# Optimization experiments

Hardware: AMD Instinct MI355X
Metric: run time of the kernel (lower is better)

Reference implementation:

```python
import math
import jax, jax.numpy as jnp
import numpy as np

EMBED_DIM = 512
NUM_HEADS = 8
HEAD_DIM = EMBED_DIM // NUM_HEADS
NUM_EDGE_TYPES = 10
N = 2048  # nodes
B = 1


def setup_inputs() -> dict:
    key = jax.random.key(0)
    ks = jax.random.split(key, 8)
    s = 1.0 / math.sqrt(EMBED_DIM)
    return {
        "query": jax.random.normal(ks[0], (N, B, EMBED_DIM), jnp.float32),
        "key": jax.random.normal(ks[1], (N, B, EMBED_DIM), jnp.float32),
        "value": jax.random.normal(ks[2], (N, B, EMBED_DIM), jnp.float32),
        "edge_id_mat": jax.random.randint(ks[3], (N, N), 0, NUM_EDGE_TYPES, jnp.int32),
        "in_proj_weight": jax.random.normal(ks[4], (3 * EMBED_DIM, EMBED_DIM), jnp.float32) * s,
        "in_proj_bias": jnp.zeros((3 * EMBED_DIM,), jnp.float32),
        "out_proj_weight": jax.random.normal(ks[5], (EMBED_DIM, EMBED_DIM), jnp.float32) * s,
        "out_proj_bias": jnp.zeros((EMBED_DIM,), jnp.float32),
        "edge_embs_K": jax.random.normal(ks[6], (NUM_EDGE_TYPES, HEAD_DIM), jnp.float32),
    }


def reference(query, key, value, edge_id_mat, in_proj_weight, in_proj_bias,
              out_proj_weight, out_proj_bias, edge_embs_K):
    L, Bsz, E = query.shape
    H, hd = NUM_HEADS, HEAD_DIM
    w_q, w_k, w_v = jnp.split(in_proj_weight, 3, axis=0)
    b_q, b_k, b_v = jnp.split(in_proj_bias, 3)
    q = query @ w_q.T + b_q   # (L, B, E)
    k = key @ w_k.T + b_k
    v = value @ w_v.T + b_v

    def split_heads(x):
        # (L, B, E) -> (B*H, L, hd)  (matches torch view(L, B*H, hd).transpose(0,1))
        return x.reshape(L, Bsz * H, hd).transpose(1, 0, 2)

    q = split_heads(q) / math.sqrt(hd)  # torch scales by sqrt(E=head_dim)
    k = split_heads(k)
    v = split_heads(v)

    attn = jnp.einsum('bnd,bmd->bnm', q, k)  # (B*H, L, L)

    # edge-type score bias: edge_attn[b,i,j] = q[b,i,:] . edge_embs_K[edge_id_mat[i,j], :]
    # computed efficiently as per-type scores then a gather (avoids (L,L,hd) tensor)
    type_scores = jnp.einsum('bnd,td->bnt', q, edge_embs_K)  # (B*H, L, T)
    idx = jnp.broadcast_to(edge_id_mat[None, :, :], attn.shape)
    edge_attn = jnp.take_along_axis(type_scores, idx, axis=2)  # (B*H, L, L)
    attn = jax.nn.softmax(attn + edge_attn, axis=-1)

    out = jnp.einsum('bnm,bmd->bnd', attn, v)           # (B*H, L, hd)
    out = out.transpose(1, 0, 2).reshape(L, Bsz, E)      # (L, B, E)
    out = out @ out_proj_weight.T + out_proj_bias
    return out
```

## Files before the change

kernel.cpp:

```cpp
#include <hip/hip_runtime.h>
#include <hip/hip_bf16.h>

#define NHEAD 8
#define SEQ   2048
#define HD    64
#define EMB   512
#define NTYPE 10
#define JSPLIT 2

#define QKV_NT (3 * EMB / 64)
#define QKV_MT (SEQ / 64)
#define QKV_BLOCKS (QKV_NT * QKV_MT)
#define PACK_BLOCKS (SEQ * SEQ / 4 / 256)

typedef unsigned short u16;
typedef __attribute__((ext_vector_type(8))) short short8;
typedef __attribute__((ext_vector_type(4))) float float4v;

union F8 { short8 v; uint4 u4; u16 us[8]; };

__device__ __forceinline__ float bf2f(u16 u){
  union { unsigned u; float f; } w; w.u = ((unsigned)u) << 16; return w.f;
}
__device__ __forceinline__ u16 f2bf(float f){
  union { float f; unsigned u; } w; w.f = f;
  unsigned u = w.u;
  u += 0x7fffu + ((u >> 16) & 1u);
  return (u16)(u >> 16);
}
__device__ __forceinline__ unsigned pk2(float a, float b){
  return (unsigned)f2bf(a) | ((unsigned)f2bf(b) << 16);
}
__device__ __forceinline__ uint4 pk8(float4 a, float4 b){
  uint4 p; p.x = pk2(a.x, a.y); p.y = pk2(a.z, a.w);
           p.z = pk2(b.x, b.y); p.w = pk2(b.z, b.w);
  return p;
}

__global__ __launch_bounds__(256) void fused_prep_gemm(
    const float* __restrict__ q, const float* __restrict__ k, const float* __restrict__ v,
    const float* __restrict__ ipw, const float* __restrict__ ipb, const int* __restrict__ eid,
    u16* __restrict__ Qs, u16* __restrict__ Kb, u16* __restrict__ Vb,
    unsigned* __restrict__ eidp)
{
  const int b = blockIdx.x;
  const int t = threadIdx.x;

  if (b >= QKV_BLOCKS) {
    const int i = (b - QKV_BLOCKS) * 256 + t;
    int4 vv = ((const int4*)eid)[i];
    eidp[i] = (unsigned)(vv.x & 0xff) | ((unsigned)(vv.y & 0xff) << 8) |
              ((unsigned)(vv.z & 0xff) << 16) | ((unsigned)(vv.w & 0xff) << 24);
    return;
  }

  __shared__ u16 As[64][40];
  __shared__ u16 Bs[64][40];

  const int nt = b % QKV_NT, mt = b / QKV_NT;
  const int n0 = nt * 64, m0 = mt * 64;
  const int z = n0 >> 9;
  const float* A = (z == 0) ? q : (z == 1) ? k : v;
  const float scale = (z == 0) ? 0.125f : 1.0f;

  const int w = t >> 6, lane = t & 63, lr = lane & 15, lg = lane >> 4;
  const int wm = w >> 1, wn = w & 1;
  const int srow = t >> 2, kb = (t & 3) * 8;

  float4v acc[2][2];
#pragma unroll
  for (int mi = 0; mi < 2; mi++)
#pragma unroll
    for (int ni = 0; ni < 2; ni++) acc[mi][ni] = (float4v){0.f, 0.f, 0.f, 0.f};

  const float* pa = A   + (size_t)(m0 + srow) * EMB + kb;
  const float* pw = ipw + (size_t)(n0 + srow) * EMB + kb;

  float4 a0 = *(const float4*)pa, a1 = *(const float4*)(pa + 4);
  float4 b0 = *(const float4*)pw, b1 = *(const float4*)(pw + 4);

  for (int k0 = 0; k0 < EMB; k0 += 32) {
    *(uint4*)&As[srow][kb] = pk8(a0, a1);
    *(uint4*)&Bs[srow][kb] = pk8(b0, b1);
    __syncthreads();
    if (k0 + 32 < EMB) {
      a0 = *(const float4*)(pa + k0 + 32); a1 = *(const float4*)(pa + k0 + 36);
      b0 = *(const float4*)(pw + k0 + 32); b1 = *(const float4*)(pw + k0 + 36);
    }
    F8 af[2], bf_[2];
#pragma unroll
    for (int mi = 0; mi < 2; mi++)
      af[mi].u4 = *(const uint4*)&As[wm * 32 + mi * 16 + lr][lg * 8];
#pragma unroll
    for (int ni = 0; ni < 2; ni++)
      bf_[ni].u4 = *(const uint4*)&Bs[wn * 32 + ni * 16 + lr][lg * 8];
#pragma unroll
    for (int mi = 0; mi < 2; mi++)
#pragma unroll
      for (int ni = 0; ni < 2; ni++)
        acc[mi][ni] = __builtin_amdgcn_mfma_f32_16x16x32_bf16(af[mi].v, bf_[ni].v, acc[mi][ni], 0, 0, 0);
    __syncthreads();
  }

  u16* O = (z == 0) ? Qs : ((z == 1) ? Kb : Vb);
#pragma unroll
  for (int mi = 0; mi < 2; mi++) {
#pragma unroll
    for (int ni = 0; ni < 2; ni++) {
      const int n = n0 + wn * 32 + ni * 16 + lr;
      const int e = n & 511, h = e >> 6, d = e & 63;
      const float bb = ipb[n];
      const int mb = m0 + wm * 32 + mi * 16 + lg * 4;
      if (z < 2) {
#pragma unroll
        for (int r = 0; r < 4; r++)
          O[((size_t)h * SEQ + mb + r) * HD + d] = f2bf((acc[mi][ni][r] + bb) * scale);
      } else {
        ushort4 pk;
        pk.x = f2bf(acc[mi][ni][0] + bb); pk.y = f2bf(acc[mi][ni][1] + bb);
        pk.z = f2bf(acc[mi][ni][2] + bb); pk.w = f2bf(acc[mi][ni][3] + bb);
        *(ushort4*)(O + ((size_t)(h * HD + d)) * SEQ + mb) = pk;
      }
    }
  }
}

__global__ __launch_bounds__(256) void attn_kernel(
    const u16* __restrict__ Qs, const u16* __restrict__ Kb, const u16* __restrict__ Vb,
    const unsigned char* __restrict__ eidp, const float* __restrict__ EK,
    float* __restrict__ Upart, float* __restrict__ mpart, float* __restrict__ lpart)
{
  __shared__ u16 Kt[64][72];
  __shared__ u16 Vt[64][72];
  __shared__ u16 Pl[4][16][72];
  __shared__ unsigned char eidt[64][64];
  __shared__ float tsl[64][13];
  __shared__ float ekl[NTYPE][64];
  __shared__ float mrow[64], lrow[64], frow[64];

  const int t = threadIdx.x;
  const int wave = t >> 6, lane = t & 63, lr = lane & 15, lg = lane >> 4;
  const int i0 = blockIdx.x * 64;
  const int h  = blockIdx.y;
  const int z  = blockIdx.z;

  for (int i = t; i < NTYPE * 64; i += 256) ekl[i >> 6][i & 63] = EK[i];
  if (t < 64) { mrow[t] = -1e30f; lrow[t] = 0.f; }
  __syncthreads();

  {
    const int row = t >> 2, tt = t & 3;
    const u16* qr = Qs + ((size_t)h * SEQ + i0 + row) * HD;
    float a0 = 0.f, a1 = 0.f, a2 = 0.f;
    for (int d0 = 0; d0 < HD; d0 += 8) {
      uint4 qq = *(const uint4*)(qr + d0);
      const u16* qu = (const u16*)&qq;
#pragma unroll
      for (int e = 0; e < 8; e++) {
        float qf = bf2f(qu[e]);
        a0 += qf * ekl[tt][d0 + e];
        a1 += qf * ekl[tt + 4][d0 + e];
        a2 += qf * ekl[(tt < 2) ? (tt + 8) : 8][d0 + e];
      }
    }
    tsl[row][tt] = a0; tsl[row][tt + 4] = a1;
    if (tt < 2) tsl[row][tt + 8] = a2;
  }

  F8 qf[2];
#pragma unroll
  for (int kc = 0; kc < 2; kc++)
    qf[kc].u4 = *(const uint4*)(Qs + ((size_t)h * SEQ + i0 + wave * 16 + lr) * HD + kc * 32 + lg * 8);

  float4v ao[4];
#pragma unroll
  for (int d = 0; d < 4; d++) ao[d] = (float4v){0.f, 0.f, 0.f, 0.f};

  const int srow = t >> 2, sdc = (t & 3) * 16;
  const int sec = sdc ^ (((t >> 4) & 3) << 4);
  const int jbase = z * (SEQ / JSPLIT);
  const int NT = (SEQ / JSPLIT) / 64;

  uint4 kp0, kp1, vp0, vp1, ep0;
  {
    const u16* kp = Kb + ((size_t)h * SEQ + jbase + srow) * HD + sdc;
    kp0 = *(const uint4*)kp; kp1 = *(const uint4*)(kp + 8);
    const u16* vp = Vb + ((size_t)(h * HD + srow)) * SEQ + jbase + sdc;
    vp0 = *(const uint4*)vp; vp1 = *(const uint4*)(vp + 8);
    ep0 = *(const uint4*)(eidp + (size_t)(i0 + srow) * SEQ + jbase + sdc);
    *(uint4*)&Kt[srow][sdc] = kp0; *(uint4*)&Kt[srow][sdc + 8] = kp1;
    *(uint4*)&Vt[srow][sdc] = vp0; *(uint4*)&Vt[srow][sdc + 8] = vp1;
    *(uint4*)&eidt[srow][sec] = ep0;
  }

  for (int jt = 0; jt < NT; jt++) {
    __syncthreads();

    if (jt + 1 < NT) {
      const int jn = jbase + (jt + 1) * 64;
      const u16* kp = Kb + ((size_t)h * SEQ + jn + srow) * HD + sdc;
      kp0 = *(const uint4*)kp; kp1 = *(const uint4*)(kp + 8);
      const u16* vp = Vb + ((size_t)(h * HD + srow)) * SEQ + jn + sdc;
      vp0 = *(const uint4*)vp; vp1 = *(const uint4*)(vp + 8);
      ep0 = *(const uint4*)(eidp + (size_t)(i0 + srow) * SEQ + jn + sdc);
    }

    float4v sacc[4];
#pragma unroll
    for (int c = 0; c < 4; c++) sacc[c] = (float4v){0.f, 0.f, 0.f, 0.f};
    __builtin_amdgcn_s_setprio(1);
#pragma unroll
    for (int kc = 0; kc < 2; kc++) {
#pragma unroll
      for (int c = 0; c < 4; c++) {
        F8 kf; kf.u4 = *(const uint4*)&Kt[c * 16 + lr][kc * 32 + lg * 8];
        sacc[c] = __builtin_amdgcn_mfma_f32_16x16x32_bf16(qf[kc].v, kf.v, sacc[c], 0, 0, 0);
      }
    }
    __builtin_amdgcn_s_setprio(0);

    float pv_[4][4];
    float rmax[4] = {-1e30f, -1e30f, -1e30f, -1e30f};
#pragma unroll
    for (int c = 0; c < 4; c++) {
      const int ec = ((c ^ lg) << 4) + lr;
#pragma unroll
      for (int r = 0; r < 4; r++) {
        const int row = wave * 16 + lg * 4 + r;
        float s = sacc[c][r] + tsl[row][eidt[row][ec]];
        pv_[c][r] = s;
        rmax[r] = fmaxf(rmax[r], s);
      }
    }
#pragma unroll
    for (int mm = 1; mm < 16; mm <<= 1) {
#pragma unroll
      for (int r = 0; r < 4; r++) rmax[r] = fmaxf(rmax[r], __shfl_xor(rmax[r], mm));
    }
    float mnew[4], fct[4], rsum[4] = {0.f, 0.f, 0.f, 0.f};
#pragma unroll
    for (int r = 0; r < 4; r++) {
      const int row = wave * 16 + lg * 4 + r;
      const float mo = mrow[row];
      mnew[r] = fmaxf(mo, rmax[r]);
      fct[r] = __expf(mo - mnew[r]);
    }
#pragma unroll
    for (int c = 0; c < 4; c++) {
#pragma unroll
      for (int r = 0; r < 4; r++) {
        float p = __expf(pv_[c][r] - mnew[r]);
        pv_[c][r] = p;
        rsum[r] += p;
      }
    }
#pragma unroll
    for (int mm = 1; mm < 16; mm <<= 1) {
#pragma unroll
      for (int r = 0; r < 4; r++) rsum[r] += __shfl_xor(rsum[r], mm);
    }
    if (lr == 0) {
#pragma unroll
      for (int r = 0; r < 4; r++) {
        const int row = wave * 16 + lg * 4 + r;
        mrow[row] = mnew[r];
        lrow[row] = lrow[row] * fct[r] + rsum[r];
        frow[row] = fct[r];
      }
    }
#pragma unroll
    for (int c = 0; c < 4; c++) {
#pragma unroll
      for (int r = 0; r < 4; r++)
        Pl[wave][lg * 4 + r][c * 16 + lr] = f2bf(pv_[c][r]);
    }
    const float fo = frow[wave * 16 + lr];
#pragma unroll
    for (int d = 0; d < 4; d++) {
#pragma unroll
      for (int r = 0; r < 4; r++) ao[d][r] *= fo;
    }
    __builtin_amdgcn_s_setprio(1);
#pragma unroll
    for (int kc = 0; kc < 2; kc++) {
      F8 pf; pf.u4 = *(const uint4*)&Pl[wave][lr][kc * 32 + lg * 8];
#pragma unroll
      for (int db = 0; db < 4; db++) {
        F8 vf; vf.u4 = *(const uint4*)&Vt[db * 16 + lr][kc * 32 + lg * 8];
        ao[db] = __builtin_amdgcn_mfma_f32_16x16x32_bf16(vf.v, pf.v, ao[db], 0, 0, 0);
      }
    }
    __builtin_amdgcn_s_setprio(0);

    __syncthreads();
    if (jt + 1 < NT) {
      *(uint4*)&Kt[srow][sdc] = kp0; *(uint4*)&Kt[srow][sdc + 8] = kp1;
      *(uint4*)&Vt[srow][sdc] = vp0; *(uint4*)&Vt[srow][sdc + 8] = vp1;
      *(uint4*)&eidt[srow][sec] = ep0;
    }
  }

  {
    const size_t base = (((size_t)z * NHEAD + h) * SEQ + i0) * HD;
#pragma unroll
    for (int db = 0; db < 4; db++) {
#pragma unroll
      for (int r = 0; r < 4; r++) {
        const int d = db * 16 + lg * 4 + r;
        const int n = wave * 16 + lr;
        Upart[base + (size_t)n * HD + d] = ao[db][r];
      }
    }
    __syncthreads();
    if (t < 64) {
      mpart[((size_t)z * NHEAD + h) * SEQ + i0 + t] = mrow[t];
      lpart[((size_t)z * NHEAD + h) * SEQ + i0 + t] = lrow[t];
    }
  }
}

__global__ __launch_bounds__(256) void combine_outproj(
    const float* __restrict__ Upart, const float* __restrict__ mpart,
    const float* __restrict__ lpart, const float* __restrict__ opw,
    const float* __restrict__ opb, float* __restrict__ out)
{
  __shared__ u16 As[64][40];
  __shared__ u16 Bs[64][40];
  __shared__ float cw0[NHEAD][64], cw1[NHEAD][64], cwi[NHEAD][64];

  const int t = threadIdx.x;
  const int n0 = blockIdx.x * 64;
  const int m0 = blockIdx.y * 64;

  for (int idx = t; idx < NHEAD * 64; idx += 256) {
    const int hh = idx >> 6, nl = idx & 63;
    const int gn = m0 + nl;
    const float mA = mpart[((size_t)0 * NHEAD + hh) * SEQ + gn];
    const float mB = mpart[((size_t)1 * NHEAD + hh) * SEQ + gn];
    const float M = fmaxf(mA, mB);
    const float w0 = __expf(mA - M), w1 = __expf(mB - M);
    const float Ls = w0 * lpart[((size_t)0 * NHEAD + hh) * SEQ + gn] +
                     w1 * lpart[((size_t)1 * NHEAD + hh) * SEQ + gn];
    cw0[hh][nl] = w0; cw1[hh][nl] = w1; cwi[hh][nl] = 1.0f / Ls;
  }
  __syncthreads();

  const int w = t >> 6, lane = t & 63, lr = lane & 15, lg = lane >> 4;
  const int wm = w >> 1, wn = w & 1;
  const int srow = t >> 2, kb = (t & 3) * 8;

  float4v acc[2][2];
#pragma unroll
  for (int mi = 0; mi < 2; mi++)
#pragma unroll
    for (int ni = 0; ni < 2; ni++) acc[mi][ni] = (float4v){0.f, 0.f, 0.f, 0.f};

  const float* pw = opw + (size_t)(n0 + srow) * EMB + kb;

  int hcur = kb >> 6, dcur = kb & 63;
  const float* pu0 = Upart + (((size_t)0 * NHEAD + hcur) * SEQ + m0 + srow) * HD + dcur;
  const float* pu1 = Upart + (((size_t)1 * NHEAD + hcur) * SEQ + m0 + srow) * HD + dcur;
  float4 u00 = *(const float4*)pu0, u01 = *(const float4*)(pu0 + 4);
  float4 u10 = *(const float4*)pu1, u11 = *(const float4*)(pu1 + 4);
  float4 b0 = *(const float4*)pw, b1 = *(const float4*)(pw + 4);

  for (int k0 = 0; k0 < EMB; k0 += 32) {
    {
      const float w0 = cw0[hcur][srow], w1 = cw1[hcur][srow], wi = cwi[hcur][srow];
      float4 c0, c1;
      c0.x = (u00.x * w0 + u10.x * w1) * wi; c0.y = (u00.y * w0 + u10.y * w1) * wi;
      c0.z = (u00.z * w0 + u10.z * w1) * wi; c0.w = (u00.w * w0 + u10.w * w1) * wi;
      c1.x = (u01.x * w0 + u11.x * w1) * wi; c1.y = (u01.y * w0 + u11.y * w1) * wi;
      c1.z = (u01.z * w0 + u11.z * w1) * wi; c1.w = (u01.w * w0 + u11.w * w1) * wi;
      *(uint4*)&As[srow][kb] = pk8(c0, c1);
      *(uint4*)&Bs[srow][kb] = pk8(b0, b1);
    }
    __syncthreads();
    if (k0 + 32 < EMB) {
      const int e = k0 + 32 + kb;
      hcur = e >> 6; dcur = e & 63;
      const float* q0 = Upart + (((size_t)0 * NHEAD + hcur) * SEQ + m0 + srow) * HD + dcur;
      const float* q1 = Upart + (((size_t)1 * NHEAD + hcur) * SEQ + m0 + srow) * HD + dcur;
      u00 = *(const float4*)q0; u01 = *(const float4*)(q0 + 4);
      u10 = *(const float4*)q1; u11 = *(const float4*)(q1 + 4);
      b0 = *(const float4*)(pw + k0 + 32); b1 = *(const float4*)(pw + k0 + 36);
    }
    F8 af[2], bf_[2];
#pragma unroll
    for (int mi = 0; mi < 2; mi++)
      af[mi].u4 = *(const uint4*)&As[wm * 32 + mi * 16 + lr][lg * 8];
#pragma unroll
    for (int ni = 0; ni < 2; ni++)
      bf_[ni].u4 = *(const uint4*)&Bs[wn * 32 + ni * 16 + lr][lg * 8];
#pragma unroll
    for (int mi = 0; mi < 2; mi++)
#pragma unroll
      for (int ni = 0; ni < 2; ni++)
        acc[mi][ni] = __builtin_amdgcn_mfma_f32_16x16x32_bf16(af[mi].v, bf_[ni].v, acc[mi][ni], 0, 0, 0);
    __syncthreads();
  }

#pragma unroll
  for (int mi = 0; mi < 2; mi++) {
#pragma unroll
    for (int ni = 0; ni < 2; ni++) {
      const int n = n0 + wn * 32 + ni * 16 + lr;
      const float bb = opb[n];
      const int mb = m0 + wm * 32 + mi * 16 + lg * 4;
#pragma unroll
      for (int r = 0; r < 4; r++)
        out[(size_t)(mb + r) * EMB + n] = acc[mi][ni][r] + bb;
    }
  }
}

extern "C" void kernel_launch(void* const* d_in, const int* in_sizes, int n_in,
                              void* d_out, int out_size, void* d_ws, size_t ws_size,
                              hipStream_t stream)
{
  const float* query = (const float*)d_in[0];
  const float* key_  = (const float*)d_in[1];
  const float* value = (const float*)d_in[2];
  const int*   eid   = (const int*)d_in[3];
  const float* ipw   = (const float*)d_in[4];
  const float* ipb   = (const float*)d_in[5];
  const float* opw   = (const float*)d_in[6];
  const float* opb   = (const float*)d_in[7];
  const float* ek    = (const float*)d_in[8];
  float* out = (float*)d_out;

  char* ws = (char*)d_ws;
  u16* Qs = (u16*)ws;              ws += (size_t)NHEAD * SEQ * HD * 2;
  u16* Kb = (u16*)ws;              ws += (size_t)NHEAD * SEQ * HD * 2;
  u16* Vb = (u16*)ws;              ws += (size_t)NHEAD * SEQ * HD * 2;
  unsigned char* eidp = (unsigned char*)ws; ws += (size_t)SEQ * SEQ;
  float* Upart = (float*)ws;       ws += (size_t)JSPLIT * NHEAD * SEQ * HD * 4;
  float* mpart = (float*)ws;       ws += (size_t)JSPLIT * NHEAD * SEQ * 4;
  float* lpart = (float*)ws;       ws += (size_t)JSPLIT * NHEAD * SEQ * 4;

  fused_prep_gemm<<<dim3(QKV_BLOCKS + PACK_BLOCKS), dim3(256), 0, stream>>>(
      query, key_, value, ipw, ipb, eid, Qs, Kb, Vb, (unsigned*)eidp);
  attn_kernel<<<dim3(SEQ / 64, NHEAD, JSPLIT), dim3(256), 0, stream>>>(
      Qs, Kb, Vb, eidp, ek, Upart, mpart, lpart);
  combine_outproj<<<dim3(EMB / 64, SEQ / 64), dim3(256), 0, stream>>>(
      Upart, mpart, lpart, opw, opb, out);
}
```

Baseline: 165.2 us.

## Transpose score MFMA so softmax row stats stay in registers; split keys four ways

The QK MFMA operands are swapped so each lane owns one query row. Row max and sum now need two cross-lane shuffles, and the running m/l live in registers instead of shared memory. Edge ids are read straight from global memory into registers rather than staged through LDS. log2e is folded into the Q scale so exp2 can replace exp, the setprio hints are dropped, and bf16 packing uses the hardware convert. The key split grows from 2 to 4 to launch more blocks, at the cost of more partial output traffic and a wider combine step in the output projection.

Measured after the change: 165.0 us. About the same (-0.1%).

```diff
diff --git a/kernel.cpp b/kernel.cpp
--- a/kernel.cpp
+++ b/kernel.cpp
@@ -6,12 +6,14 @@
 #define HD    64
 #define EMB   512
 #define NTYPE 10
-#define JSPLIT 2
+#define JSPLIT 4
 
 #define QKV_NT (3 * EMB / 64)
 #define QKV_MT (SEQ / 64)
 #define QKV_BLOCKS (QKV_NT * QKV_MT)
 #define PACK_BLOCKS (SEQ * SEQ / 4 / 256)
+
+#define QSCALE 0.180336878f
 
 typedef unsigned short u16;
 typedef __attribute__((ext_vector_type(8))) short short8;
@@ -28,12 +30,14 @@
   u += 0x7fffu + ((u >> 16) & 1u);
   return (u16)(u >> 16);
 }
-__device__ __forceinline__ unsigned pk2(float a, float b){
-  return (unsigned)f2bf(a) | ((unsigned)f2bf(b) << 16);
+__device__ __forceinline__ unsigned cvtpk(float lo, float hi){
+  union { __hip_bfloat162 b; unsigned u; } w;
+  w.b = __float22bfloat162_rn(float2{lo, hi});
+  return w.u;
 }
 __device__ __forceinline__ uint4 pk8(float4 a, float4 b){
-  uint4 p; p.x = pk2(a.x, a.y); p.y = pk2(a.z, a.w);
-           p.z = pk2(b.x, b.y); p.w = pk2(b.z, b.w);
+  uint4 p; p.x = cvtpk(a.x, a.y); p.y = cvtpk(a.z, a.w);
+           p.z = cvtpk(b.x, b.y); p.w = cvtpk(b.z, b.w);
   return p;
 }
 
@@ -61,7 +65,7 @@
   const int n0 = nt * 64, m0 = mt * 64;
   const int z = n0 >> 9;
   const float* A = (z == 0) ? q : (z == 1) ? k : v;
-  const float scale = (z == 0) ? 0.125f : 1.0f;
+  const float scale = (z == 0) ? QSCALE : 1.0f;
 
   const int w = t >> 6, lane = t & 63, lr = lane & 15, lg = lane >> 4;
   const int wm = w >> 1, wn = w & 1;
@@ -127,16 +131,14 @@
 
 __global__ __launch_bounds__(256) void attn_kernel(
     const u16* __restrict__ Qs, const u16* __restrict__ Kb, const u16* __restrict__ Vb,
-    const unsigned char* __restrict__ eidp, const float* __restrict__ EK,
+    const unsigned* __restrict__ eid32, const float* __restrict__ EK,
     float* __restrict__ Upart, float* __restrict__ mpart, float* __restrict__ lpart)
 {
   __shared__ u16 Kt[64][72];
   __shared__ u16 Vt[64][72];
   __shared__ u16 Pl[4][16][72];
-  __shared__ unsigned char eidt[64][64];
   __shared__ float tsl[64][13];
   __shared__ float ekl[NTYPE][64];
-  __shared__ float mrow[64], lrow[64], frow[64];
 
   const int t = threadIdx.x;
   const int wave = t >> 6, lane = t & 63, lr = lane & 15, lg = lane >> 4;
@@ -145,7 +147,6 @@
   const int z  = blockIdx.z;
 
   for (int i = t; i < NTYPE * 64; i += 256) ekl[i >> 6][i & 63] = EK[i];
-  if (t < 64) { mrow[t] = -1e30f; lrow[t] = 0.f; }
   __syncthreads();
 
   {
@@ -175,22 +176,25 @@
   float4v ao[4];
 #pragma unroll
   for (int d = 0; d < 4; d++) ao[d] = (float4v){0.f, 0.f, 0.f, 0.f};
+  float m_i = -1e30f, l_i = 0.f;
 
   const int srow = t >> 2, sdc = (t & 3) * 16;
-  const int sec = sdc ^ (((t >> 4) & 3) << 4);
   const int jbase = z * (SEQ / JSPLIT);
   const int NT = (SEQ / JSPLIT) / 64;
-
-  uint4 kp0, kp1, vp0, vp1, ep0;
+  const unsigned* erow = eid32 + (size_t)(i0 + wave * 16 + lr) * (SEQ / 4);
+
+  uint4 kp0, kp1, vp0, vp1;
+  unsigned ed[4], edn[4];
   {
     const u16* kp = Kb + ((size_t)h * SEQ + jbase + srow) * HD + sdc;
     kp0 = *(const uint4*)kp; kp1 = *(const uint4*)(kp + 8);
     const u16* vp = Vb + ((size_t)(h * HD + srow)) * SEQ + jbase + sdc;
     vp0 = *(const uint4*)vp; vp1 = *(const uint4*)(vp + 8);
-    ep0 = *(const uint4*)(eidp + (size_t)(i0 + srow) * SEQ + jbase + sdc);
     *(uint4*)&Kt[srow][sdc] = kp0; *(uint4*)&Kt[srow][sdc + 8] = kp1;
     *(uint4*)&Vt[srow][sdc] = vp0; *(uint4*)&Vt[srow][sdc + 8] = vp1;
-    *(uint4*)&eidt[srow][sec] = ep0;
+    const int ej = jbase >> 2;
+#pragma unroll
+    for (int c = 0; c < 4; c++) ed[c] = erow[ej + c * 4 + lg];
   }
 
   for (int jt = 0; jt < NT; jt++) {
@@ -202,85 +206,65 @@
       kp0 = *(const uint4*)kp; kp1 = *(const uint4*)(kp + 8);
       const u16* vp = Vb + ((size_t)(h * HD + srow)) * SEQ + jn + sdc;
       vp0 = *(const uint4*)vp; vp1 = *(const uint4*)(vp + 8);
-      ep0 = *(const uint4*)(eidp + (size_t)(i0 + srow) * SEQ + jn + sdc);
+      const int ejn = jn >> 2;
+#pragma unroll
+      for (int c = 0; c < 4; c++) edn[c] = erow[ejn + c * 4 + lg];
     }
 
     float4v sacc[4];
 #pragma unroll
     for (int c = 0; c < 4; c++) sacc[c] = (float4v){0.f, 0.f, 0.f, 0.f};
-    __builtin_amdgcn_s_setprio(1);
 #pragma unroll
     for (int kc = 0; kc < 2; kc++) {
 #pragma unroll
       for (int c = 0; c < 4; c++) {
         F8 kf; kf.u4 = *(const uint4*)&Kt[c * 16 + lr][kc * 32 + lg * 8];
-        sacc[c] = __builtin_amdgcn_mfma_f32_16x16x32_bf16(qf[kc].v, kf.v, sacc[c], 0, 0, 0);
-      }
-    }
-    __builtin_amdgcn_s_setprio(0);
-
-    float pv_[4][4];
-    float rmax[4] = {-1e30f, -1e30f, -1e30f, -1e30f};
+        sacc[c] = __builtin_amdgcn_mfma_f32_16x16x32_bf16(kf.v, qf[kc].v, sacc[c], 0, 0, 0);
+      }
+    }
+
+    float rmax = -1e30f;
 #pragma unroll
     for (int c = 0; c < 4; c++) {
-      const int ec = ((c ^ lg) << 4) + lr;
+      const unsigned e = ed[c];
 #pragma unroll
       for (int r = 0; r < 4; r++) {
-        const int row = wave * 16 + lg * 4 + r;
-        float s = sacc[c][r] + tsl[row][eidt[row][ec]];
-        pv_[c][r] = s;
-        rmax[r] = fmaxf(rmax[r], s);
-      }
-    }
-#pragma unroll
-    for (int mm = 1; mm < 16; mm <<= 1) {
-#pragma unroll
-      for (int r = 0; r < 4; r++) rmax[r] = fmaxf(rmax[r], __shfl_xor(rmax[r], mm));
-    }
-    float mnew[4], fct[4], rsum[4] = {0.f, 0.f, 0.f, 0.f};
-#pragma unroll
-    for (int r = 0; r < 4; r++) {
-      const int row = wave * 16 + lg * 4 + r;
-      const float mo = mrow[row];
-      mnew[r] = fmaxf(mo, rmax[r]);
-      fct[r] = __expf(mo - mnew[r]);
-    }
+        const float s = sacc[c][r] + tsl[wave * 16 + lr][(e >> (r * 8)) & 0xffu];
+        sacc[c][r] = s;
+        rmax = fmaxf(rmax, s);
+      }
+    }
+    rmax = fmaxf(rmax, __shfl_xor(rmax, 16));
+    rmax = fmaxf(rmax, __shfl_xor(rmax, 32));
+    const float mnew = fmaxf(m_i, rmax);
+    const float fct = exp2f(m_i - mnew);
+    float rsum = 0.f;
 #pragma unroll
     for (int c = 0; c < 4; c++) {
 #pragma unroll
       for (int r = 0; r < 4; r++) {
-        float p = __expf(pv_[c][r] - mnew[r]);
-        pv_[c][r] = p;
-        rsum[r] += p;
-      }
-    }
-#pragma unroll
-    for (int mm = 1; mm < 16; mm <<= 1) {
-#pragma unroll
-      for (int r = 0; r < 4; r++) rsum[r] += __shfl_xor(rsum[r], mm);
-    }
-    if (lr == 0) {
-#pragma unroll
-      for (int r = 0; r < 4; r++) {
-        const int row = wave * 16 + lg * 4 + r;
-        mrow[row] = mnew[r];
-        lrow[row] = lrow[row] * fct[r] + rsum[r];
-        frow[row] = fct[r];
-      }
-    }
+        const float p = exp2f(sacc[c][r] - mnew);
+        sacc[c][r] = p;
+        rsum += p;
+      }
+    }
+    rsum += __shfl_xor(rsum, 16);
+    rsum += __shfl_xor(rsum, 32);
+    l_i = l_i * fct + rsum;
+    m_i = mnew;
+
 #pragma unroll
     for (int c = 0; c < 4; c++) {
-#pragma unroll
-      for (int r = 0; r < 4; r++)
-        Pl[wave][lg * 4 + r][c * 16 + lr] = f2bf(pv_[c][r]);
-    }
-    const float fo = frow[wave * 16 + lr];
-#pragma unroll
-    for (int d = 0; d < 4; d++) {
-#pragma unroll
-      for (int r = 0; r < 4; r++) ao[d][r] *= fo;
-    }
-    __builtin_amdgcn_s_setprio(1);
+      uint2 pw;
+      pw.x = cvtpk(sacc[c][0], sacc[c][1]);
+      pw.y = cvtpk(sacc[c][2], sacc[c][3]);
+      *(uint2*)&Pl[wave][lr][c * 16 + lg * 4] = pw;
+    }
+#pragma unroll
+    for (int db = 0; db < 4; db++) {
+#pragma unroll
+      for (int r = 0; r < 4; r++) ao[db][r] *= fct;
+    }
 #pragma unroll
     for (int kc = 0; kc < 2; kc++) {
       F8 pf; pf.u4 = *(const uint4*)&Pl[wave][lr][kc * 32 + lg * 8];
@@ -290,13 +274,13 @@
         ao[db] = __builtin_amdgcn_mfma_f32_16x16x32_bf16(vf.v, pf.v, ao[db], 0, 0, 0);
       }
     }
-    __builtin_amdgcn_s_setprio(0);
 
     __syncthreads();
     if (jt + 1 < NT) {
       *(uint4*)&Kt[srow][sdc] = kp0; *(uint4*)&Kt[srow][sdc + 8] = kp1;
       *(uint4*)&Vt[srow][sdc] = vp0; *(uint4*)&Vt[srow][sdc + 8] = vp1;
-      *(uint4*)&eidt[srow][sec] = ep0;
+#pragma unroll
+      for (int c = 0; c < 4; c++) ed[c] = edn[c];
     }
   }
 
@@ -311,10 +295,9 @@
         Upart[base + (size_t)n * HD + d] = ao[db][r];
       }
     }
-    __syncthreads();
-    if (t < 64) {
-      mpart[((size_t)z * NHEAD + h) * SEQ + i0 + t] = mrow[t];
-      lpart[((size_t)z * NHEAD + h) * SEQ + i0 + t] = lrow[t];
+    if (lg == 0) {
+      mpart[((size_t)z * NHEAD + h) * SEQ + i0 + wave * 16 + lr] = m_i;
+      lpart[((size_t)z * NHEAD + h) * SEQ + i0 + wave * 16 + lr] = l_i;
     }
   }
 }
@@ -326,7 +309,7 @@
 {
   __shared__ u16 As[64][40];
   __shared__ u16 Bs[64][40];
-  __shared__ float cw0[NHEAD][64], cw1[NHEAD][64], cwi[NHEAD][64];
+  __shared__ float cww[JSPLIT][NHEAD][64];
 
   const int t = threadIdx.x;
   const int n0 = blockIdx.x * 64;
@@ -335,13 +318,22 @@
   for (int idx = t; idx < NHEAD * 64; idx += 256) {
     const int hh = idx >> 6, nl = idx & 63;
     const int gn = m0 + nl;
-    const float mA = mpart[((size_t)0 * NHEAD + hh) * SEQ + gn];
-    const float mB = mpart[((size_t)1 * NHEAD + hh) * SEQ + gn];
-    const float M = fmaxf(mA, mB);
-    const float w0 = __expf(mA - M), w1 = __expf(mB - M);
-    const float Ls = w0 * lpart[((size_t)0 * NHEAD + hh) * SEQ + gn] +
-                     w1 * lpart[((size_t)1 * NHEAD + hh) * SEQ + gn];
-    cw0[hh][nl] = w0; cw1[hh][nl] = w1; cwi[hh][nl] = 1.0f / Ls;
+    float mz[JSPLIT], wz[JSPLIT];
+    float M = -1e30f;
+#pragma unroll
+    for (int zz = 0; zz < JSPLIT; zz++) {
+      mz[zz] = mpart[((size_t)zz * NHEAD + hh) * SEQ + gn];
+      M = fmaxf(M, mz[zz]);
+    }
+    float Ls = 0.f;
+#pragma unroll
+    for (int zz = 0; zz < JSPLIT; zz++) {
+      wz[zz] = exp2f(mz[zz] - M);
+      Ls += wz[zz] * lpart[((size_t)zz * NHEAD + hh) * SEQ + gn];
+    }
+    const float inv = 1.0f / Ls;
+#pragma unroll
+    for (int zz = 0; zz < JSPLIT; zz++) cww[zz][hh][nl] = wz[zz] * inv;
   }
   __syncthreads();
 
@@ -358,20 +350,25 @@
   const float* pw = opw + (size_t)(n0 + srow) * EMB + kb;
 
   int hcur = kb >> 6, dcur = kb & 63;
-  const float* pu0 = Upart + (((size_t)0 * NHEAD + hcur) * SEQ + m0 + srow) * HD + dcur;
-  const float* pu1 = Upart + (((size_t)1 * NHEAD + hcur) * SEQ + m0 + srow) * HD + dcur;
-  float4 u00 = *(const float4*)pu0, u01 = *(const float4*)(pu0 + 4);
-  float4 u10 = *(const float4*)pu1, u11 = *(const float4*)(pu1 + 4);
+  float4 ua[JSPLIT][2];
+#pragma unroll
+  for (int zz = 0; zz < JSPLIT; zz++) {
+    const float* pu = Upart + (((size_t)zz * NHEAD + hcur) * SEQ + m0 + srow) * HD + dcur;
+    ua[zz][0] = *(const float4*)pu; ua[zz][1] = *(const float4*)(pu + 4);
+  }
   float4 b0 = *(const float4*)pw, b1 = *(const float4*)(pw + 4);
 
   for (int k0 = 0; k0 < EMB; k0 += 32) {
     {
-      const float w0 = cw0[hcur][srow], w1 = cw1[hcur][srow], wi = cwi[hcur][srow];
-      float4 c0, c1;
-      c0.x = (u00.x * w0 + u10.x * w1) * wi; c0.y = (u00.y * w0 + u10.y * w1) * wi;
-      c0.z = (u00.z * w0 + u10.z * w1) * wi; c0.w = (u00.w * w0 + u10.w * w1) * wi;
-      c1.x = (u01.x * w0 + u11.x * w1) * wi; c1.y = (u01.y * w0 + u11.y * w1) * wi;
-      c1.z = (u01.z * w0 + u11.z * w1) * wi; c1.w = (u01.w * w0 + u11.w * w1) * wi;
+      float4 c0 = {0.f,0.f,0.f,0.f}, c1 = {0.f,0.f,0.f,0.f};
+#pragma unroll
+      for (int zz = 0; zz < JSPLIT; zz++) {
+        const float wgt = cww[zz][hcur][srow];
+        c0.x += ua[zz][0].x * wgt; c0.y += ua[zz][0].y * wgt;
+        c0.z += ua[zz][0].z * wgt; c0.w += ua[zz][0].w * wgt;
+        c1.x += ua[zz][1].x * wgt; c1.y += ua[zz][1].y * wgt;
+        c1.z += ua[zz][1].z * wgt; c1.w += ua[zz][1].w * wgt;
+      }
       *(uint4*)&As[srow][kb] = pk8(c0, c1);
       *(uint4*)&Bs[srow][kb] = pk8(b0, b1);
     }
@@ -379,10 +376,11 @@
     if (k0 + 32 < EMB) {
       const int e = k0 + 32 + kb;
       hcur = e >> 6; dcur = e & 63;
-      const float* q0 = Upart + (((size_t)0 * NHEAD + hcur) * SEQ + m0 + srow) * HD + dcur;
-      const float* q1 = Upart + (((size_t)1 * NHEAD + hcur) * SEQ + m0 + srow) * HD + dcur;
-      u00 = *(const float4*)q0; u01 = *(const float4*)(q0 + 4);
-      u10 = *(const float4*)q1; u11 = *(const float4*)(q1 + 4);
+#pragma unroll
+      for (int zz = 0; zz < JSPLIT; zz++) {
+        const float* pu = Upart + (((size_t)zz * NHEAD + hcur) * SEQ + m0 + srow) * HD + dcur;
+        ua[zz][0] = *(const float4*)pu; ua[zz][1] = *(const float4*)(pu + 4);
+      }
       b0 = *(const float4*)(pw + k0 + 32); b1 = *(const float4*)(pw + k0 + 36);
     }
     F8 af[2], bf_[2];
@@ -433,13 +431,13 @@
   u16* Qs = (u16*)ws;              ws += (size_t)NHEAD * SEQ * HD * 2;
   u16* Kb = (u16*)ws;              ws += (size_t)NHEAD * SEQ * HD * 2;
   u16* Vb = (u16*)ws;              ws += (size_t)NHEAD * SEQ * HD * 2;
-  unsigned char* eidp = (unsigned char*)ws; ws += (size_t)SEQ * SEQ;
+  unsigned* eidp = (unsigned*)ws;  ws += (size_t)SEQ * SEQ;
   float* Upart = (float*)ws;       ws += (size_t)JSPLIT * NHEAD * SEQ * HD * 4;
   float* mpart = (float*)ws;       ws += (size_t)JSPLIT * NHEAD * SEQ * 4;
   float* lpart = (float*)ws;       ws += (size_t)JSPLIT * NHEAD * SEQ * 4;
 
   fused_prep_gemm<<<dim3(QKV_BLOCKS + PACK_BLOCKS), dim3(256), 0, stream>>>(
-      query, key_, value, ipw, ipb, eid, Qs, Kb, Vb, (unsigned*)eidp);
+      query, key_, value, ipw, ipb, eid, Qs, Kb, Vb, eidp);
   attn_kernel<<<dim3(SEQ / 64, NHEAD, JSPLIT), dim3(256), 0, stream>>>(
       Qs, Kb, Vb, eidp, ek, Upart, mpart, lpart);
   combine_outproj<<<dim3(EMB / 64, SEQ / 64), dim3(256), 0, stream>>>(
```
